# Kernel tuning notes

Hardware: AMD Instinct MI355X
Metric: run time of the kernel (lower is better)

## Reference

```python
import jax, jax.numpy as jnp
import numpy as np

N = 50000          # masked node count
E = 800000         # edges (avg degree 16)
IN_DIM, GCN_DIM, REL_DIM, TRAIN_DIM, OUT_DIM = 3, 128, 64, 128, 2
BATCHES = 1


def setup_inputs() -> dict:
    key = jax.random.key(0)
    ks = jax.random.split(key, 16)
    s = 0.05
    return {
        "features": jax.random.normal(ks[0], (N, IN_DIM), jnp.float32),
        "edge_index": jax.random.randint(ks[1], (2, E), 0, N, dtype=jnp.int32),
        "trainOT": jax.random.normal(ks[2], (TRAIN_DIM,), jnp.float32),
        "W1": jax.random.normal(ks[3], (IN_DIM, GCN_DIM), jnp.float32) * s,
        "b1": jnp.zeros((GCN_DIM,), jnp.float32),
        "W2": jax.random.normal(ks[4], (GCN_DIM, GCN_DIM), jnp.float32) * s,
        "b2": jnp.zeros((GCN_DIM,), jnp.float32),
        "Wq": jax.random.normal(ks[5], (GCN_DIM, REL_DIM), jnp.float32) * s,
        "bq": jnp.zeros((REL_DIM,), jnp.float32),
        "Wk": jax.random.normal(ks[6], (TRAIN_DIM, REL_DIM), jnp.float32) * s,
        "bk": jnp.zeros((REL_DIM,), jnp.float32),
        "Wv": jax.random.normal(ks[7], (GCN_DIM, TRAIN_DIM), jnp.float32) * s,
        "bv": jnp.zeros((TRAIN_DIM,), jnp.float32),
        "Ws": jax.random.normal(ks[8], (TRAIN_DIM, OUT_DIM * N), jnp.float32) * s,
        "bs": jnp.zeros((OUT_DIM * N,), jnp.float32),
    }


def _gcn_conv(x, W, b, src, dst, n):
    """PyG GCNConv: h = D^-1/2 (A+I) D^-1/2 (x W) + b (self-loops already in src/dst)."""
    h = x @ W                                                  # [n, d_out]
    ones = jnp.ones(src.shape[0], dtype=x.dtype)
    deg = jax.ops.segment_sum(ones, dst, num_segments=n)      # in-degree incl. self-loop
    dinv = jnp.where(deg > 0, jax.lax.rsqrt(deg), 0.0)
    norm = dinv[src] * dinv[dst]                               # [E+n]
    msg = h[src] * norm[:, None]                               # gather (dominant traffic)
    return jax.ops.segment_sum(msg, dst, num_segments=n) + b   # scatter-add


def reference(features, edge_index, trainOT, W1, b1, W2, b2, Wq, bq, Wk, bk, Wv, bv, Ws, bs):
    n = features.shape[0]
    loop = jnp.arange(n, dtype=edge_index.dtype)
    src = jnp.concatenate([edge_index[0], loop])
    dst = jnp.concatenate([edge_index[1], loop])

    h1 = jax.nn.relu(_gcn_conv(features, W1, b1, src, dst, n))   # gcn1 + relu
    h2 = _gcn_conv(h1, W2, b2, src, dst, n)                      # gcn2

    q = h2 @ Wq + bq                                             # [n, rel]
    v = h2 @ Wv + bv                                             # [n, train]
    k = trainOT @ Wk + bk                                        # [rel]
    scale = jnp.asarray(Wq.shape[1], q.dtype) ** 0.5
    rel = jax.nn.sigmoid((q @ k) / scale)                        # [n]
    summed_idea = (rel[:, None] * v).sum(axis=0)                 # [train]
    new_trainOT = trainOT + summed_idea
    speak = new_trainOT @ Ws + bs                                # [out_dim * num_nodes]
    out = speak.reshape(BATCHES, -1, OUT_DIM)
    return out, new_trainOT
```

## Files before the change

### kernel.cpp

```cpp
#include <hip/hip_runtime.h>
#include <math.h>

#define O_RPD    (0)
#define O_RPS    (256*1024)
#define O_DINV   (512*1024)
#define O_SMALL  (768*1024)
#define O_Y      (1024*1024)
#define O_RELW   (1280*1024)
#define O_REL    (1536*1024)
#define O_GHD    (1792*1024)
#define O_GHS    (2048*1024)
#define O_GOD    (2304*1024)
#define O_GOS    (2560*1024)
#define O_BSD    (2816*1024)
#define O_BSS    (2944*1024)
#define O_PART   (3072*1024)
#define O_XS     (3712*1024)
#define O_SRTD   (4608*1024)
#define O_SRTS   (11776*1024 - 3584*1024)
#define O_COLD   (11776*1024)
#define O_COLS   (15360*1024)
#define O_H1     (18688*1024)

#define NCHUNK 256
#define ZBLOCKS 1024

static __device__ __forceinline__ unsigned int f2bf(float f) {
    unsigned int u = __float_as_uint(f);
    return (u + 0x7fffu + ((u >> 16) & 1u)) >> 16;
}
static __device__ __forceinline__ float bf_lo(unsigned int w) { return __uint_as_float(w << 16); }
static __device__ __forceinline__ float bf_hi(unsigned int w) { return __uint_as_float(w & 0xffff0000u); }

static __device__ __forceinline__ int blockExclScan256(int v, volatile int* lds, int t) {
    int lane = t & 63, wid = t >> 6;
    int incl = v;
#pragma unroll
    for (int off = 1; off < 64; off <<= 1) {
        int n = __shfl_up(incl, off);
        if (lane >= off) incl += n;
    }
    if (lane == 63) lds[wid] = incl;
    __syncthreads();
    if (t == 0) {
        int s = 0;
#pragma unroll
        for (int i = 0; i < 4; ++i) { int x = lds[i]; lds[i] = s; s += x; }
    }
    __syncthreads();
    return lds[wid] + incl - v;
}

__global__ void k_hist(const int* __restrict__ eidx, int* __restrict__ ghD,
                       int* __restrict__ ghS, int E, int CS, int NB) {
    __shared__ int lh[256];
    int b = blockIdx.x, t = threadIdx.x;
    const int* arr = blockIdx.y ? eidx : (eidx + E);
    int* gh = blockIdx.y ? ghS : ghD;
    lh[t] = 0; __syncthreads();
    int s = b * CS, e = min(E, s + CS);
    for (int i = s + t; i < e; i += 256) atomicAdd(&lh[arr[i] >> 8], 1);
    __syncthreads();
    if (t < NB) gh[t * NCHUNK + b] = lh[t];
}

__global__ void k_bstart(const int* __restrict__ ghD, const int* __restrict__ ghS,
                         int* __restrict__ bsD, int* __restrict__ bsS, int NB) {
    __shared__ int lds1[4];
    __shared__ int lds2[4];
    int t = threadIdx.x;
    int vD = 0, vS = 0;
    if (t < NB) {
        const int* rD = ghD + t * NCHUNK;
        const int* rS = ghS + t * NCHUNK;
        for (int b = 0; b < NCHUNK; ++b) { vD += rD[b]; vS += rS[b]; }
    }
    int exD = blockExclScan256(vD, lds1, t);
    if (t <= NB) bsD[t] = exD;
    __syncthreads();
    int exS = blockExclScan256(vS, lds2, t);
    if (t <= NB) bsS[t] = exS;
}

__global__ void k_goff(const int* __restrict__ ghD, const int* __restrict__ ghS,
                       const int* __restrict__ bsD, const int* __restrict__ bsS,
                       int* __restrict__ goD, int* __restrict__ goS, int NB) {
    __shared__ int lds1[4];
    int nb = blockIdx.x, t = threadIdx.x;
    const int* gh = blockIdx.y ? ghS : ghD;
    const int* bs = blockIdx.y ? bsS : bsD;
    int* go = blockIdx.y ? goS : goD;
    int base = bs[nb];
    int g = gh[nb * NCHUNK + t];
    int gx = blockExclScan256(g, lds1, t);
    go[nb * NCHUNK + t] = base + gx;
}

__global__ void k_scatter(const int* __restrict__ eidx, const int* __restrict__ goD,
                          const int* __restrict__ goS, unsigned int* __restrict__ srtD,
                          unsigned int* __restrict__ srtS, int E, int CS, int NB) {
    __shared__ int lcur[256];
    int b = blockIdx.x, t = threadIdx.x;
    const int* key = blockIdx.y ? eidx : (eidx + E);
    const int* val = blockIdx.y ? (eidx + E) : eidx;
    const int* go  = blockIdx.y ? goS : goD;
    unsigned int* srt = blockIdx.y ? srtS : srtD;
    if (t < NB) lcur[t] = go[t * NCHUNK + b];
    __syncthreads();
    int s = b * CS, e = min(E, s + CS);
    for (int i = s + t; i < e; i += 256) {
        int k = key[i];
        int pos = atomicAdd(&lcur[k >> 8], 1);
        srt[pos] = ((unsigned int)(k & 255) << 16) | (unsigned int)val[i];
    }
}

__global__ void k_build(const unsigned int* __restrict__ srtD, const unsigned int* __restrict__ srtS,
                        const int* __restrict__ bsD, const int* __restrict__ bsS,
                        int* __restrict__ rpD, int* __restrict__ rpS,
                        int* __restrict__ colD, int* __restrict__ colS,
                        float* __restrict__ dinv, const float* __restrict__ x,
                        float4* __restrict__ xs4, const float* __restrict__ bs,
                        float* __restrict__ out, int N, int NB) {
    __shared__ int lcnt[256];
    __shared__ int lpos[256];
    __shared__ int lds1[4];
    int nb = blockIdx.x, t = threadIdx.x;
    bool rev = blockIdx.y != 0;
    const unsigned int* srt = rev ? srtS : srtD;
    const int* bst = rev ? bsS : bsD;
    int* rp  = rev ? rpS : rpD;
    int* col = rev ? colS : colD;
    lcnt[t] = 0; __syncthreads();
    int s = bst[nb], e = bst[nb + 1];
    for (int i = s + t; i < e; i += 256) atomicAdd(&lcnt[srt[i] >> 16], 1);
    __syncthreads();
    int c = lcnt[t];
    int cx = blockExclScan256(c, lds1, t);
    int rpv = s + cx;
    int node = (nb << 8) + t;
    rp[node] = rpv;
    lpos[t] = rpv;
    if (!rev && node < N) {
        float d = rsqrtf((float)(c + 1));
        dinv[node] = d;
        float4 v;
        v.x = x[node * 3] * d; v.y = x[node * 3 + 1] * d; v.z = x[node * 3 + 2] * d; v.w = 0.f;
        xs4[node] = v;
        reinterpret_cast<float2*>(out)[node] = reinterpret_cast<const float2*>(bs)[node];
    }
    __syncthreads();
    for (int i = s + t; i < e; i += 256) {
        unsigned int v = srt[i];
        int p = atomicAdd(&lpos[v >> 16], 1);
        col[p] = (int)(v & 0xffffu);
    }
}

__global__ void k_tiny1(const float* __restrict__ trainOT, const float* __restrict__ Wq,
                        const float* __restrict__ bq, const float* __restrict__ Wk,
                        const float* __restrict__ bk, const float* __restrict__ W2,
                        const float* __restrict__ b2, float* __restrict__ small) {
    __shared__ float kv[64];
    __shared__ float wqk[128];
    __shared__ float red[128];
    int t = threadIdx.x;
    if (t < 64) {
        float acc = bk[t];
        for (int j = 0; j < 128; ++j) acc += trainOT[j] * Wk[j * 64 + t];
        kv[t] = acc;
    }
    __syncthreads();
    float accq = 0.f;
    for (int c = 0; c < 64; ++c) accq += Wq[t * 64 + c] * kv[c];
    wqk[t] = accq;
    red[t] = (t < 64) ? bq[t] * kv[t] : 0.f;
    __syncthreads();
    for (int off = 64; off >= 1; off >>= 1) { if (t < off) red[t] += red[t + off]; __syncthreads(); }
    float bqs = red[0];
    __syncthreads();
    float acc2 = 0.f;
    for (int j = 0; j < 128; ++j) acc2 += W2[t * 128 + j] * wqk[j];
    small[t] = acc2;
    red[t] = b2[t] * wqk[t];
    __syncthreads();
    for (int off = 64; off >= 1; off >>= 1) { if (t < off) red[t] += red[t + off]; __syncthreads(); }
    if (t == 0) small[128] = bqs + red[0];
}

__global__ void k_layer1(const float4* __restrict__ xs4, const int* __restrict__ rpD,
                         const int* __restrict__ colD, const float* __restrict__ dinv,
                         const float* __restrict__ W1, const float* __restrict__ b1,
                         const float* __restrict__ small, unsigned int* __restrict__ h1s,
                         float* __restrict__ y, int N) {
    int t = threadIdx.x;
    int sub = t & 15;
    int node = blockIdx.x * 16 + (t >> 4);
    if (node >= N) return;
    float di = dinv[node];
    int s = rpD[node], e = rpD[node + 1];
    float a0 = 0.f, a1 = 0.f, a2 = 0.f;
    for (int j = s + sub; j < e; j += 16) {
        float4 xv = xs4[colD[j]];
        a0 += xv.x; a1 += xv.y; a2 += xv.z;
    }
    if (sub == 0) { float4 xv = xs4[node]; a0 += xv.x; a1 += xv.y; a2 += xv.z; }
#pragma unroll
    for (int off = 1; off < 16; off <<= 1) {
        a0 += __shfl_xor(a0, off);
        a1 += __shfl_xor(a1, off);
        a2 += __shfl_xor(a2, off);
    }
    a0 *= di; a1 *= di; a2 *= di;
    unsigned int p[4];
    float yl = 0.f;
#pragma unroll
    for (int m = 0; m < 4; ++m) {
        int c = 8 * sub + 2 * m;
        float vlo = fmaxf(a0 * W1[c]     + a1 * W1[128 + c]     + a2 * W1[256 + c]     + b1[c],     0.f) * di;
        float vhi = fmaxf(a0 * W1[c + 1] + a1 * W1[128 + c + 1] + a2 * W1[256 + c + 1] + b1[c + 1], 0.f) * di;
        p[m] = f2bf(vlo) | (f2bf(vhi) << 16);
        yl += bf_lo(p[m]) * small[c] + bf_hi(p[m]) * small[c + 1];
    }
    uint4 st; st.x = p[0]; st.y = p[1]; st.z = p[2]; st.w = p[3];
    reinterpret_cast<uint4*>(h1s + (size_t)node * 64)[sub] = st;
#pragma unroll
    for (int off = 1; off < 16; off <<= 1) yl += __shfl_xor(yl, off);
    if (sub == 0) y[node] = yl;
}

__global__ void k_dv(const float* __restrict__ y, const int* __restrict__ rpD,
                     const int* __restrict__ colD, const float* __restrict__ dinv,
                     const float* __restrict__ small, float* __restrict__ relw,
                     float* __restrict__ rel, int N) {
    int t = threadIdx.x;
    int sub = t & 15;
    int node = blockIdx.x * 16 + (t >> 4);
    if (node >= N) return;
    float di = dinv[node];
    int s = rpD[node], e = rpD[node + 1];
    float acc = (sub == 0) ? y[node] : 0.f;
    for (int j = s + sub; j < e; j += 16) acc += y[colD[j]];
#pragma unroll
    for (int off = 1; off < 16; off <<= 1) acc += __shfl_xor(acc, off);
    float z = (acc * di + small[128]) * 0.125f;
    float r = 1.f / (1.f + __expf(-z));
    if (sub == 0) { rel[node] = r; relw[node] = r * di; }
}

__global__ void k_z(const unsigned int* __restrict__ h1s, const int* __restrict__ rpS,
                    const int* __restrict__ colS, const float* __restrict__ relw,
                    const float* __restrict__ rel, float* __restrict__ part, int N) {
    int t = threadIdx.x, lane = t & 63, wid = t >> 6;
    int sub = lane & 15;
    float acc[8];
#pragma unroll
    for (int j = 0; j < 8; ++j) acc[j] = 0.f;
    float Racc = 0.f;
    for (int node = blockIdx.x * 16 + (t >> 4); node < N; node += ZBLOCKS * 16) {
        int s = rpS[node], e = rpS[node + 1];
        float w = (sub == 0) ? relw[node] : 0.f;
        for (int j = s + sub; j < e; j += 16) w += relw[colS[j]];
#pragma unroll
        for (int off = 1; off < 16; off <<= 1) w += __shfl_xor(w, off);
        uint4 v = reinterpret_cast<const uint4*>(h1s + (size_t)node * 64)[sub];
        acc[0] += w * bf_lo(v.x); acc[1] += w * bf_hi(v.x);
        acc[2] += w * bf_lo(v.y); acc[3] += w * bf_hi(v.y);
        acc[4] += w * bf_lo(v.z); acc[5] += w * bf_hi(v.z);
        acc[6] += w * bf_lo(v.w); acc[7] += w * bf_hi(v.w);
        if (sub == 0) Racc += rel[node];
    }
#pragma unroll
    for (int j = 0; j < 8; ++j) {
        acc[j] += __shfl_xor(acc[j], 16);
        acc[j] += __shfl_xor(acc[j], 32);
    }
    Racc += __shfl_xor(Racc, 16);
    Racc += __shfl_xor(Racc, 32);
    __shared__ float sS[4][132];
    if (lane < 16) {
#pragma unroll
        for (int j = 0; j < 8; ++j) sS[wid][8 * sub + j] = acc[j];
    }
    if (lane == 0) sS[wid][128] = Racc;
    __syncthreads();
    if (t < 129) part[blockIdx.x * 132 + t] = sS[0][t] + sS[1][t] + sS[2][t] + sS[3][t];
}

__global__ void k_reduce_part(const float* __restrict__ part, int nblocks, float* __restrict__ small) {
    int c = blockIdx.x;
    float acc = 0.f;
    for (int b = threadIdx.x; b < nblocks; b += blockDim.x) acc += part[b * 132 + c];
    __shared__ float sd[256];
    sd[threadIdx.x] = acc; __syncthreads();
    for (int off = 128; off; off >>= 1) { if (threadIdx.x < off) sd[threadIdx.x] += sd[threadIdx.x + off]; __syncthreads(); }
    if (threadIdx.x == 0) small[132 + c] = sd[0];
}

__global__ void k_tiny2(const float* __restrict__ trainOT, const float* __restrict__ W2,
                        const float* __restrict__ b2, const float* __restrict__ Wv,
                        const float* __restrict__ bv, float* __restrict__ small,
                        float* __restrict__ out_tail) {
    __shared__ float t1[128];
    int t = threadIdx.x;
    float R = small[260];
    float acc = R * b2[t];
    for (int j = 0; j < 128; ++j) acc += small[132 + j] * W2[j * 128 + t];
    t1[t] = acc; __syncthreads();
    float acc2 = R * bv[t];
    for (int j = 0; j < 128; ++j) acc2 += t1[j] * Wv[j * 128 + t];
    float nt = trainOT[t] + acc2;
    small[264 + t] = nt;
    out_tail[t] = nt;
}

__global__ void k_tail(const float* __restrict__ Ws, const float* __restrict__ small,
                       float* __restrict__ out, int out_n) {
    int ks = blockIdx.x & 3;
    int j = ((blockIdx.x >> 2) << 8) + threadIdx.x;
    if (j >= out_n) return;
    const float* w = Ws + (size_t)(ks * 32) * out_n + j;
    const float* nt = small + 264 + ks * 32;
    float acc = 0.f;
#pragma unroll 8
    for (int k = 0; k < 32; ++k) acc += nt[k] * w[(size_t)k * out_n];
    atomicAdd(&out[j], acc);
}

extern "C" void kernel_launch(void* const* d_in, const int* in_sizes, int n_in,
                              void* d_out, int out_size, void* d_ws, size_t ws_size,
                              hipStream_t stream) {
    const float* features = (const float*)d_in[0];
    const int*   eidx     = (const int*)d_in[1];
    const float* trainOT  = (const float*)d_in[2];
    const float* W1 = (const float*)d_in[3];
    const float* b1 = (const float*)d_in[4];
    const float* W2 = (const float*)d_in[5];
    const float* b2 = (const float*)d_in[6];
    const float* Wq = (const float*)d_in[7];
    const float* bq = (const float*)d_in[8];
    const float* Wk = (const float*)d_in[9];
    const float* bk = (const float*)d_in[10];
    const float* Wv = (const float*)d_in[11];
    const float* bv = (const float*)d_in[12];
    const float* Ws = (const float*)d_in[13];
    const float* bs = (const float*)d_in[14];

    int N = in_sizes[0] / 3;
    int E = in_sizes[1] / 2;
    int NB = (N + 255) >> 8;
    int CS = (E + NCHUNK - 1) / NCHUNK;

    char* ws = (char*)d_ws;
    int*   rpD   = (int*)(ws + O_RPD);
    int*   rpS   = (int*)(ws + O_RPS);
    float* dinv  = (float*)(ws + O_DINV);
    float* small = (float*)(ws + O_SMALL);
    float* y     = (float*)(ws + O_Y);
    float* relw  = (float*)(ws + O_RELW);
    float* rel   = (float*)(ws + O_REL);
    int*   ghD   = (int*)(ws + O_GHD);
    int*   ghS   = (int*)(ws + O_GHS);
    int*   goD   = (int*)(ws + O_GOD);
    int*   goS   = (int*)(ws + O_GOS);
    int*   bsD   = (int*)(ws + O_BSD);
    int*   bsS   = (int*)(ws + O_BSS);
    float* part  = (float*)(ws + O_PART);
    float4* xs4  = (float4*)(ws + O_XS);
    unsigned int* srtD = (unsigned int*)(ws + O_SRTD);
    unsigned int* srtS = (unsigned int*)(ws + O_SRTS);
    int*   colD  = (int*)(ws + O_COLD);
    int*   colS  = (int*)(ws + O_COLS);
    unsigned int* h1s = (unsigned int*)(ws + O_H1);
    float* out   = (float*)d_out;
    int out_n = out_size - 128;

    k_tiny1<<<1, 128, 0, stream>>>(trainOT, Wq, bq, Wk, bk, W2, b2, small);
    k_hist<<<dim3(NCHUNK, 2), 256, 0, stream>>>(eidx, ghD, ghS, E, CS, NB);
    k_bstart<<<1, 256, 0, stream>>>(ghD, ghS, bsD, bsS, NB);
    k_goff<<<dim3(NB, 2), 256, 0, stream>>>(ghD, ghS, bsD, bsS, goD, goS, NB);
    k_scatter<<<dim3(NCHUNK, 2), 256, 0, stream>>>(eidx, goD, goS, srtD, srtS, E, CS, NB);
    k_build<<<dim3(NB, 2), 256, 0, stream>>>(srtD, srtS, bsD, bsS, rpD, rpS, colD, colS,
                                             dinv, features, xs4, bs, out, N, NB);
    k_layer1<<<(N + 15) / 16, 256, 0, stream>>>(xs4, rpD, colD, dinv, W1, b1, small, h1s, y, N);
    k_dv<<<(N + 15) / 16, 256, 0, stream>>>(y, rpD, colD, dinv, small, relw, rel, N);
    k_z<<<ZBLOCKS, 256, 0, stream>>>(h1s, rpS, colS, relw, rel, part, N);
    k_reduce_part<<<129, 256, 0, stream>>>(part, ZBLOCKS, small);
    k_tiny2<<<1, 128, 0, stream>>>(trainOT, W2, b2, Wv, bv, small, out + out_n);
    k_tail<<<((out_n + 255) / 256) * 4, 256, 0, stream>>>(Ws, small, out, out_n);
}
```

Measured before the change: 113.0 us.

## Aggregate directly from bucket-sorted edges with LDS atomics, dropping CSR build

Removes the per-node CSR construction (row pointers and column arrays) and instead aggregates over the 256-node bucket-sorted edge lists with shared-memory atomics per block. The bf16 h1 buffer is no longer stored. Layer-1 activations are recomputed from a compact per-node float4 of pre-activation inputs and dinv. The separate partial-reduce kernel is folded into k_tiny2, and the rel sum moves into k_dv. This cuts global traffic and launches, at the cost of LDS atomic contention, recomputing h1, and a serial reduction over blocks in a single-block kernel.

```diff
diff --git a/kernel.cpp b/kernel.cpp
--- a/kernel.cpp
+++ b/kernel.cpp
@@ -1,36 +1,23 @@
 #include <hip/hip_runtime.h>
 #include <math.h>
 
-#define O_RPD    (0)
-#define O_RPS    (256*1024)
-#define O_DINV   (512*1024)
-#define O_SMALL  (768*1024)
-#define O_Y      (1024*1024)
-#define O_RELW   (1280*1024)
-#define O_REL    (1536*1024)
-#define O_GHD    (1792*1024)
-#define O_GHS    (2048*1024)
-#define O_GOD    (2304*1024)
-#define O_GOS    (2560*1024)
-#define O_BSD    (2816*1024)
-#define O_BSS    (2944*1024)
-#define O_PART   (3072*1024)
-#define O_XS     (3712*1024)
-#define O_SRTD   (4608*1024)
-#define O_SRTS   (11776*1024 - 3584*1024)
-#define O_COLD   (11776*1024)
-#define O_COLS   (15360*1024)
-#define O_H1     (18688*1024)
+#define O_SMALL  (0)
+#define O_DINV   (256*1024)
+#define O_Y      (512*1024)
+#define O_RELW   (768*1024)
+#define O_PART   (1024*1024)
+#define O_GHD    (1536*1024)
+#define O_GHS    (1792*1024)
+#define O_GOD    (2048*1024)
+#define O_GOS    (2304*1024)
+#define O_BSD    (2560*1024)
+#define O_BSS    (2688*1024)
+#define O_XS     (2816*1024)
+#define O_G1     (3840*1024)
+#define O_SRTD   (4864*1024)
+#define O_SRTS   (8192*1024)
 
 #define NCHUNK 256
-#define ZBLOCKS 1024
-
-static __device__ __forceinline__ unsigned int f2bf(float f) {
-    unsigned int u = __float_as_uint(f);
-    return (u + 0x7fffu + ((u >> 16) & 1u)) >> 16;
-}
-static __device__ __forceinline__ float bf_lo(unsigned int w) { return __uint_as_float(w << 16); }
-static __device__ __forceinline__ float bf_hi(unsigned int w) { return __uint_as_float(w & 0xffff0000u); }
 
 static __device__ __forceinline__ int blockExclScan256(int v, volatile int* lds, int t) {
     int lane = t & 63, wid = t >> 6;
@@ -115,45 +102,24 @@
     }
 }
 
-__global__ void k_build(const unsigned int* __restrict__ srtD, const unsigned int* __restrict__ srtS,
-                        const int* __restrict__ bsD, const int* __restrict__ bsS,
-                        int* __restrict__ rpD, int* __restrict__ rpS,
-                        int* __restrict__ colD, int* __restrict__ colS,
-                        float* __restrict__ dinv, const float* __restrict__ x,
-                        float4* __restrict__ xs4, const float* __restrict__ bs,
-                        float* __restrict__ out, int N, int NB) {
+__global__ void k_prep(const unsigned int* __restrict__ srtD, const int* __restrict__ bsD,
+                       const float* __restrict__ x, const float* __restrict__ bs,
+                       float* __restrict__ out, float* __restrict__ dinv,
+                       float4* __restrict__ xs4, int N) {
     __shared__ int lcnt[256];
-    __shared__ int lpos[256];
-    __shared__ int lds1[4];
-    int nb = blockIdx.x, t = threadIdx.x;
-    bool rev = blockIdx.y != 0;
-    const unsigned int* srt = rev ? srtS : srtD;
-    const int* bst = rev ? bsS : bsD;
-    int* rp  = rev ? rpS : rpD;
-    int* col = rev ? colS : colD;
+    int nb = blockIdx.x, t = threadIdx.x;
     lcnt[t] = 0; __syncthreads();
-    int s = bst[nb], e = bst[nb + 1];
-    for (int i = s + t; i < e; i += 256) atomicAdd(&lcnt[srt[i] >> 16], 1);
-    __syncthreads();
-    int c = lcnt[t];
-    int cx = blockExclScan256(c, lds1, t);
-    int rpv = s + cx;
+    int s = bsD[nb], e = bsD[nb + 1];
+    for (int i = s + t; i < e; i += 256) atomicAdd(&lcnt[srtD[i] >> 16], 1);
+    __syncthreads();
     int node = (nb << 8) + t;
-    rp[node] = rpv;
-    lpos[t] = rpv;
-    if (!rev && node < N) {
-        float d = rsqrtf((float)(c + 1));
+    if (node < N) {
+        float d = rsqrtf((float)(lcnt[t] + 1));
         dinv[node] = d;
         float4 v;
         v.x = x[node * 3] * d; v.y = x[node * 3 + 1] * d; v.z = x[node * 3 + 2] * d; v.w = 0.f;
         xs4[node] = v;
         reinterpret_cast<float2*>(out)[node] = reinterpret_cast<const float2*>(bs)[node];
-    }
-    __syncthreads();
-    for (int i = s + t; i < e; i += 256) {
-        unsigned int v = srt[i];
-        int p = atomicAdd(&lpos[v >> 16], 1);
-        col[p] = (int)(v & 0xffffu);
     }
 }
 
@@ -188,124 +154,155 @@
     if (t == 0) small[128] = bqs + red[0];
 }
 
-__global__ void k_layer1(const float4* __restrict__ xs4, const int* __restrict__ rpD,
-                         const int* __restrict__ colD, const float* __restrict__ dinv,
-                         const float* __restrict__ W1, const float* __restrict__ b1,
-                         const float* __restrict__ small, unsigned int* __restrict__ h1s,
-                         float* __restrict__ y, int N) {
-    int t = threadIdx.x;
-    int sub = t & 15;
-    int node = blockIdx.x * 16 + (t >> 4);
-    if (node >= N) return;
-    float di = dinv[node];
-    int s = rpD[node], e = rpD[node + 1];
-    float a0 = 0.f, a1 = 0.f, a2 = 0.f;
-    for (int j = s + sub; j < e; j += 16) {
-        float4 xv = xs4[colD[j]];
-        a0 += xv.x; a1 += xv.y; a2 += xv.z;
-    }
-    if (sub == 0) { float4 xv = xs4[node]; a0 += xv.x; a1 += xv.y; a2 += xv.z; }
-#pragma unroll
-    for (int off = 1; off < 16; off <<= 1) {
-        a0 += __shfl_xor(a0, off);
-        a1 += __shfl_xor(a1, off);
-        a2 += __shfl_xor(a2, off);
-    }
-    a0 *= di; a1 *= di; a2 *= di;
-    unsigned int p[4];
-    float yl = 0.f;
-#pragma unroll
-    for (int m = 0; m < 4; ++m) {
-        int c = 8 * sub + 2 * m;
-        float vlo = fmaxf(a0 * W1[c]     + a1 * W1[128 + c]     + a2 * W1[256 + c]     + b1[c],     0.f) * di;
-        float vhi = fmaxf(a0 * W1[c + 1] + a1 * W1[128 + c + 1] + a2 * W1[256 + c + 1] + b1[c + 1], 0.f) * di;
-        p[m] = f2bf(vlo) | (f2bf(vhi) << 16);
-        yl += bf_lo(p[m]) * small[c] + bf_hi(p[m]) * small[c + 1];
-    }
-    uint4 st; st.x = p[0]; st.y = p[1]; st.z = p[2]; st.w = p[3];
-    reinterpret_cast<uint4*>(h1s + (size_t)node * 64)[sub] = st;
-#pragma unroll
-    for (int off = 1; off < 16; off <<= 1) yl += __shfl_xor(yl, off);
-    if (sub == 0) y[node] = yl;
-}
-
-__global__ void k_dv(const float* __restrict__ y, const int* __restrict__ rpD,
-                     const int* __restrict__ colD, const float* __restrict__ dinv,
+__global__ void k_y(const unsigned int* __restrict__ srtD, const int* __restrict__ bsD,
+                    const float4* __restrict__ xs4, const float* __restrict__ dinv,
+                    const float* __restrict__ W1, const float* __restrict__ b1,
+                    const float* __restrict__ small, float4* __restrict__ g1,
+                    float* __restrict__ y, int N) {
+    __shared__ float ax[256], ay[256], az[256];
+    __shared__ float W1s[384];
+    __shared__ float b1s[128], wqks[128];
+    int nb = blockIdx.x, t = threadIdx.x;
+    ax[t] = 0.f; ay[t] = 0.f; az[t] = 0.f;
+    if (t < 128) { W1s[t] = W1[t]; W1s[128 + t] = W1[128 + t]; W1s[256 + t] = W1[256 + t];
+                   b1s[t] = b1[t]; wqks[t] = small[t]; }
+    __syncthreads();
+    int s = bsD[nb], e = bsD[nb + 1];
+    for (int i = s + t; i < e; i += 256) {
+        unsigned int v = srtD[i];
+        int d = v >> 16;
+        float4 xv = xs4[v & 0xffffu];
+        atomicAdd(&ax[d], xv.x); atomicAdd(&ay[d], xv.y); atomicAdd(&az[d], xv.z);
+    }
+    __syncthreads();
+    int grp = t >> 4, sub = t & 15;
+#pragma unroll 4
+    for (int r = 0; r < 16; ++r) {
+        int nl = r * 16 + grp;
+        int node = (nb << 8) + nl;
+        float a0 = 0.f, a1 = 0.f, a2 = 0.f, di = 0.f, yl = 0.f;
+        if (node < N) {
+            di = dinv[node];
+            float4 self = xs4[node];
+            a0 = (ax[nl] + self.x) * di;
+            a1 = (ay[nl] + self.y) * di;
+            a2 = (az[nl] + self.z) * di;
+#pragma unroll
+            for (int m = 0; m < 8; ++m) {
+                int c = sub * 8 + m;
+                float h = fmaxf(a0 * W1s[c] + a1 * W1s[128 + c] + a2 * W1s[256 + c] + b1s[c], 0.f);
+                yl += h * wqks[c];
+            }
+        }
+#pragma unroll
+        for (int off = 1; off < 16; off <<= 1) yl += __shfl_xor(yl, off);
+        if (node < N && sub == 0) {
+            y[node] = yl * di;
+            float4 gv; gv.x = a0; gv.y = a1; gv.z = a2; gv.w = di;
+            g1[node] = gv;
+        }
+    }
+}
+
+__global__ void k_dv(const unsigned int* __restrict__ srtD, const int* __restrict__ bsD,
+                     const float* __restrict__ y, const float* __restrict__ dinv,
                      const float* __restrict__ small, float* __restrict__ relw,
-                     float* __restrict__ rel, int N) {
-    int t = threadIdx.x;
-    int sub = t & 15;
-    int node = blockIdx.x * 16 + (t >> 4);
-    if (node >= N) return;
-    float di = dinv[node];
-    int s = rpD[node], e = rpD[node + 1];
-    float acc = (sub == 0) ? y[node] : 0.f;
-    for (int j = s + sub; j < e; j += 16) acc += y[colD[j]];
-#pragma unroll
-    for (int off = 1; off < 16; off <<= 1) acc += __shfl_xor(acc, off);
-    float z = (acc * di + small[128]) * 0.125f;
-    float r = 1.f / (1.f + __expf(-z));
-    if (sub == 0) { rel[node] = r; relw[node] = r * di; }
-}
-
-__global__ void k_z(const unsigned int* __restrict__ h1s, const int* __restrict__ rpS,
-                    const int* __restrict__ colS, const float* __restrict__ relw,
-                    const float* __restrict__ rel, float* __restrict__ part, int N) {
-    int t = threadIdx.x, lane = t & 63, wid = t >> 6;
-    int sub = lane & 15;
+                     float* __restrict__ part, int N) {
+    __shared__ float dvl[256];
+    __shared__ float red[256];
+    int nb = blockIdx.x, t = threadIdx.x;
+    dvl[t] = 0.f; __syncthreads();
+    int s = bsD[nb], e = bsD[nb + 1];
+    float bias = small[128];
+    for (int i = s + t; i < e; i += 256) {
+        unsigned int v = srtD[i];
+        atomicAdd(&dvl[v >> 16], y[v & 0xffffu]);
+    }
+    __syncthreads();
+    int node = (nb << 8) + t;
+    float rel = 0.f;
+    if (node < N) {
+        float di = dinv[node];
+        float dv = (dvl[t] + y[node]) * di;
+        float z = (dv + bias) * 0.125f;
+        rel = 1.f / (1.f + __expf(-z));
+        relw[node] = rel * di;
+    }
+    red[t] = rel; __syncthreads();
+    for (int off = 128; off >= 1; off >>= 1) { if (t < off) red[t] += red[t + off]; __syncthreads(); }
+    if (t == 0) part[nb * 132 + 128] = red[0];
+}
+
+__global__ void k_S(const unsigned int* __restrict__ srtS, const int* __restrict__ bsS,
+                    const float* __restrict__ relw, const float4* __restrict__ g1,
+                    const float* __restrict__ W1, const float* __restrict__ b1,
+                    float* __restrict__ part, int N) {
+    __shared__ float zl[256];
+    __shared__ float W1s[384];
+    __shared__ float b1s[128];
+    __shared__ float sS[4][128];
+    int nb = blockIdx.x, t = threadIdx.x;
+    zl[t] = 0.f;
+    if (t < 128) { W1s[t] = W1[t]; W1s[128 + t] = W1[128 + t]; W1s[256 + t] = W1[256 + t];
+                   b1s[t] = b1[t]; }
+    __syncthreads();
+    int s = bsS[nb], e = bsS[nb + 1];
+    for (int i = s + t; i < e; i += 256) {
+        unsigned int v = srtS[i];
+        atomicAdd(&zl[v >> 16], relw[v & 0xffffu]);
+    }
+    __syncthreads();
+    int grp = t >> 4, sub = t & 15, lane = t & 63, wid = t >> 6;
     float acc[8];
 #pragma unroll
-    for (int j = 0; j < 8; ++j) acc[j] = 0.f;
-    float Racc = 0.f;
-    for (int node = blockIdx.x * 16 + (t >> 4); node < N; node += ZBLOCKS * 16) {
-        int s = rpS[node], e = rpS[node + 1];
-        float w = (sub == 0) ? relw[node] : 0.f;
-        for (int j = s + sub; j < e; j += 16) w += relw[colS[j]];
-#pragma unroll
-        for (int off = 1; off < 16; off <<= 1) w += __shfl_xor(w, off);
-        uint4 v = reinterpret_cast<const uint4*>(h1s + (size_t)node * 64)[sub];
-        acc[0] += w * bf_lo(v.x); acc[1] += w * bf_hi(v.x);
-        acc[2] += w * bf_lo(v.y); acc[3] += w * bf_hi(v.y);
-        acc[4] += w * bf_lo(v.z); acc[5] += w * bf_hi(v.z);
-        acc[6] += w * bf_lo(v.w); acc[7] += w * bf_hi(v.w);
-        if (sub == 0) Racc += rel[node];
-    }
-#pragma unroll
-    for (int j = 0; j < 8; ++j) {
-        acc[j] += __shfl_xor(acc[j], 16);
-        acc[j] += __shfl_xor(acc[j], 32);
-    }
-    Racc += __shfl_xor(Racc, 16);
-    Racc += __shfl_xor(Racc, 32);
-    __shared__ float sS[4][132];
+    for (int m = 0; m < 8; ++m) acc[m] = 0.f;
+#pragma unroll 4
+    for (int r = 0; r < 16; ++r) {
+        int nl = r * 16 + grp;
+        int node = (nb << 8) + nl;
+        if (node < N) {
+            float4 gv = g1[node];
+            float zu = zl[nl] + relw[node];
+            float zw = zu * gv.w;
+#pragma unroll
+            for (int m = 0; m < 8; ++m) {
+                int c = sub * 8 + m;
+                float h = fmaxf(gv.x * W1s[c] + gv.y * W1s[128 + c] + gv.z * W1s[256 + c] + b1s[c], 0.f);
+                acc[m] += zw * h;
+            }
+        }
+    }
+#pragma unroll
+    for (int m = 0; m < 8; ++m) {
+        acc[m] += __shfl_xor(acc[m], 16);
+        acc[m] += __shfl_xor(acc[m], 32);
+    }
     if (lane < 16) {
 #pragma unroll
-        for (int j = 0; j < 8; ++j) sS[wid][8 * sub + j] = acc[j];
-    }
-    if (lane == 0) sS[wid][128] = Racc;
-    __syncthreads();
-    if (t < 129) part[blockIdx.x * 132 + t] = sS[0][t] + sS[1][t] + sS[2][t] + sS[3][t];
-}
-
-__global__ void k_reduce_part(const float* __restrict__ part, int nblocks, float* __restrict__ small) {
-    int c = blockIdx.x;
-    float acc = 0.f;
-    for (int b = threadIdx.x; b < nblocks; b += blockDim.x) acc += part[b * 132 + c];
-    __shared__ float sd[256];
-    sd[threadIdx.x] = acc; __syncthreads();
-    for (int off = 128; off; off >>= 1) { if (threadIdx.x < off) sd[threadIdx.x] += sd[threadIdx.x + off]; __syncthreads(); }
-    if (threadIdx.x == 0) small[132 + c] = sd[0];
+        for (int m = 0; m < 8; ++m) sS[wid][lane * 8 + m] = acc[m];
+    }
+    __syncthreads();
+    if (t < 128) part[nb * 132 + t] = sS[0][t] + sS[1][t] + sS[2][t] + sS[3][t];
 }
 
 __global__ void k_tiny2(const float* __restrict__ trainOT, const float* __restrict__ W2,
                         const float* __restrict__ b2, const float* __restrict__ Wv,
-                        const float* __restrict__ bv, float* __restrict__ small,
-                        float* __restrict__ out_tail) {
+                        const float* __restrict__ bv, const float* __restrict__ part,
+                        float* __restrict__ small, float* __restrict__ out_tail, int NB) {
+    __shared__ float Ss[128];
     __shared__ float t1[128];
+    __shared__ float red[128];
     int t = threadIdx.x;
-    float R = small[260];
+    float sv = 0.f;
+    for (int b = 0; b < NB; ++b) sv += part[b * 132 + t];
+    Ss[t] = sv;
+    float r = 0.f;
+    for (int b = t; b < NB; b += 128) r += part[b * 132 + 128];
+    red[t] = r; __syncthreads();
+    for (int off = 64; off >= 1; off >>= 1) { if (t < off) red[t] += red[t + off]; __syncthreads(); }
+    float R = red[0];
     float acc = R * b2[t];
-    for (int j = 0; j < 128; ++j) acc += small[132 + j] * W2[j * 128 + t];
+    for (int j = 0; j < 128; ++j) acc += Ss[j] * W2[j * 128 + t];
     t1[t] = acc; __syncthreads();
     float acc2 = R * bv[t];
     for (int j = 0; j < 128; ++j) acc2 += t1[j] * Wv[j * 128 + t];
@@ -352,26 +349,21 @@
     int CS = (E + NCHUNK - 1) / NCHUNK;
 
     char* ws = (char*)d_ws;
-    int*   rpD   = (int*)(ws + O_RPD);
-    int*   rpS   = (int*)(ws + O_RPS);
+    float* small = (float*)(ws + O_SMALL);
     float* dinv  = (float*)(ws + O_DINV);
-    float* small = (float*)(ws + O_SMALL);
     float* y     = (float*)(ws + O_Y);
     float* relw  = (float*)(ws + O_RELW);
-    float* rel   = (float*)(ws + O_REL);
+    float* part  = (float*)(ws + O_PART);
     int*   ghD   = (int*)(ws + O_GHD);
     int*   ghS   = (int*)(ws + O_GHS);
     int*   goD   = (int*)(ws + O_GOD);
     int*   goS   = (int*)(ws + O_GOS);
     int*   bsD   = (int*)(ws + O_BSD);
     int*   bsS   = (int*)(ws + O_BSS);
-    float* part  = (float*)(ws + O_PART);
     float4* xs4  = (float4*)(ws + O_XS);
+    float4* g1   = (float4*)(ws + O_G1);
     unsigned int* srtD = (unsigned int*)(ws + O_SRTD);
     unsigned int* srtS = (unsigned int*)(ws + O_SRTS);
-    int*   colD  = (int*)(ws + O_COLD);
-    int*   colS  = (int*)(ws + O_COLS);
-    unsigned int* h1s = (unsigned int*)(ws + O_H1);
     float* out   = (float*)d_out;
     int out_n = out_size - 128;
 
@@ -380,12 +372,10 @@
     k_bstart<<<1, 256, 0, stream>>>(ghD, ghS, bsD, bsS, NB);
     k_goff<<<dim3(NB, 2), 256, 0, stream>>>(ghD, ghS, bsD, bsS, goD, goS, NB);
     k_scatter<<<dim3(NCHUNK, 2), 256, 0, stream>>>(eidx, goD, goS, srtD, srtS, E, CS, NB);
-    k_build<<<dim3(NB, 2), 256, 0, stream>>>(srtD, srtS, bsD, bsS, rpD, rpS, colD, colS,
-                                             dinv, features, xs4, bs, out, N, NB);
-    k_layer1<<<(N + 15) / 16, 256, 0, stream>>>(xs4, rpD, colD, dinv, W1, b1, small, h1s, y, N);
-    k_dv<<<(N + 15) / 16, 256, 0, stream>>>(y, rpD, colD, dinv, small, relw, rel, N);
-    k_z<<<ZBLOCKS, 256, 0, stream>>>(h1s, rpS, colS, relw, rel, part, N);
-    k_reduce_part<<<129, 256, 0, stream>>>(part, ZBLOCKS, small);
-    k_tiny2<<<1, 128, 0, stream>>>(trainOT, W2, b2, Wv, bv, small, out + out_n);
+    k_prep<<<NB, 256, 0, stream>>>(srtD, bsD, features, bs, out, dinv, xs4, N);
+    k_y<<<NB, 256, 0, stream>>>(srtD, bsD, xs4, dinv, W1, b1, small, g1, y, N);
+    k_dv<<<NB, 256, 0, stream>>>(srtD, bsD, y, dinv, small, relw, part, N);
+    k_S<<<NB, 256, 0, stream>>>(srtS, bsS, relw, g1, W1, b1, part, N);
+    k_tiny2<<<1, 128, 0, stream>>>(trainOT, W2, b2, Wv, bv, part, small, out + out_n, NB);
     k_tail<<<((out_n + 255) / 256) * 4, 256, 0, stream>>>(Ws, small, out, out_n);
 }
```

Result: slower. 172.2 us (+52.4%).

## Recompute layer-1 activations in k_z instead of storing bf16 h1

Applied to the files above, without the earlier changes.

Instead of materialising the 128-wide bf16 h1 matrix per node, layer-1 stores only the aggregated 3-dim input plus dinv as a float4, and k_z recomputes relu(xW1+b1) on the fly from W1/b1 held in shared memory. This removes a large intermediate write and read (about 256 bytes per node) in exchange for extra ALU work in k_z, and it also drops the bf16 rounding. Separately, the single-block tiny matvec kernel is widened from 128 to 1024 threads, splitting the K dimension into slices and reducing through shared memory.

```diff
diff --git a/kernel.cpp b/kernel.cpp
--- a/kernel.cpp
+++ b/kernel.cpp
@@ -16,21 +16,14 @@
 #define O_BSS    (2944*1024)
 #define O_PART   (3072*1024)
 #define O_XS     (3712*1024)
-#define O_SRTD   (4608*1024)
-#define O_SRTS   (11776*1024 - 3584*1024)
-#define O_COLD   (11776*1024)
-#define O_COLS   (15360*1024)
-#define O_H1     (18688*1024)
+#define O_G1     (4608*1024)
+#define O_SRTD   (5632*1024)
+#define O_SRTS   (9216*1024)
+#define O_COLD   (12544*1024)
+#define O_COLS   (16128*1024)
 
 #define NCHUNK 256
 #define ZBLOCKS 1024
-
-static __device__ __forceinline__ unsigned int f2bf(float f) {
-    unsigned int u = __float_as_uint(f);
-    return (u + 0x7fffu + ((u >> 16) & 1u)) >> 16;
-}
-static __device__ __forceinline__ float bf_lo(unsigned int w) { return __uint_as_float(w << 16); }
-static __device__ __forceinline__ float bf_hi(unsigned int w) { return __uint_as_float(w & 0xffff0000u); }
 
 static __device__ __forceinline__ int blockExclScan256(int v, volatile int* lds, int t) {
     int lane = t & 63, wid = t >> 6;
@@ -188,11 +181,11 @@
     if (t == 0) small[128] = bqs + red[0];
 }
 
-__global__ void k_layer1(const float4* __restrict__ xs4, const int* __restrict__ rpD,
-                         const int* __restrict__ colD, const float* __restrict__ dinv,
-                         const float* __restrict__ W1, const float* __restrict__ b1,
-                         const float* __restrict__ small, unsigned int* __restrict__ h1s,
-                         float* __restrict__ y, int N) {
+__global__ void k_y(const float4* __restrict__ xs4, const int* __restrict__ rpD,
+                    const int* __restrict__ colD, const float* __restrict__ dinv,
+                    const float* __restrict__ W1, const float* __restrict__ b1,
+                    const float* __restrict__ small, float4* __restrict__ g1,
+                    float* __restrict__ y, int N) {
     int t = threadIdx.x;
     int sub = t & 15;
     int node = blockIdx.x * 16 + (t >> 4);
@@ -212,21 +205,20 @@
         a2 += __shfl_xor(a2, off);
     }
     a0 *= di; a1 *= di; a2 *= di;
-    unsigned int p[4];
     float yl = 0.f;
 #pragma unroll
-    for (int m = 0; m < 4; ++m) {
-        int c = 8 * sub + 2 * m;
-        float vlo = fmaxf(a0 * W1[c]     + a1 * W1[128 + c]     + a2 * W1[256 + c]     + b1[c],     0.f) * di;
-        float vhi = fmaxf(a0 * W1[c + 1] + a1 * W1[128 + c + 1] + a2 * W1[256 + c + 1] + b1[c + 1], 0.f) * di;
-        p[m] = f2bf(vlo) | (f2bf(vhi) << 16);
-        yl += bf_lo(p[m]) * small[c] + bf_hi(p[m]) * small[c + 1];
-    }
-    uint4 st; st.x = p[0]; st.y = p[1]; st.z = p[2]; st.w = p[3];
-    reinterpret_cast<uint4*>(h1s + (size_t)node * 64)[sub] = st;
+    for (int m = 0; m < 8; ++m) {
+        int c = sub * 8 + m;
+        float h = fmaxf(a0 * W1[c] + a1 * W1[128 + c] + a2 * W1[256 + c] + b1[c], 0.f);
+        yl += h * small[c];
+    }
 #pragma unroll
     for (int off = 1; off < 16; off <<= 1) yl += __shfl_xor(yl, off);
-    if (sub == 0) y[node] = yl;
+    if (sub == 0) {
+        y[node] = yl * di;
+        float4 gv; gv.x = a0; gv.y = a1; gv.z = a2; gv.w = di;
+        g1[node] = gv;
+    }
 }
 
 __global__ void k_dv(const float* __restrict__ y, const int* __restrict__ rpD,
@@ -248,14 +240,21 @@
     if (sub == 0) { rel[node] = r; relw[node] = r * di; }
 }
 
-__global__ void k_z(const unsigned int* __restrict__ h1s, const int* __restrict__ rpS,
+__global__ void k_z(const float4* __restrict__ g1, const int* __restrict__ rpS,
                     const int* __restrict__ colS, const float* __restrict__ relw,
-                    const float* __restrict__ rel, float* __restrict__ part, int N) {
+                    const float* __restrict__ rel, const float* __restrict__ W1,
+                    const float* __restrict__ b1, float* __restrict__ part, int N) {
+    __shared__ float W1s[384];
+    __shared__ float b1s[128];
+    __shared__ float sS[4][132];
     int t = threadIdx.x, lane = t & 63, wid = t >> 6;
     int sub = lane & 15;
+    if (t < 128) { W1s[t] = W1[t]; W1s[128 + t] = W1[128 + t]; W1s[256 + t] = W1[256 + t];
+                   b1s[t] = b1[t]; }
+    __syncthreads();
     float acc[8];
 #pragma unroll
-    for (int j = 0; j < 8; ++j) acc[j] = 0.f;
+    for (int m = 0; m < 8; ++m) acc[m] = 0.f;
     float Racc = 0.f;
     for (int node = blockIdx.x * 16 + (t >> 4); node < N; node += ZBLOCKS * 16) {
         int s = rpS[node], e = rpS[node + 1];
@@ -263,24 +262,26 @@
         for (int j = s + sub; j < e; j += 16) w += relw[colS[j]];
 #pragma unroll
         for (int off = 1; off < 16; off <<= 1) w += __shfl_xor(w, off);
-        uint4 v = reinterpret_cast<const uint4*>(h1s + (size_t)node * 64)[sub];
-        acc[0] += w * bf_lo(v.x); acc[1] += w * bf_hi(v.x);
-        acc[2] += w * bf_lo(v.y); acc[3] += w * bf_hi(v.y);
-        acc[4] += w * bf_lo(v.z); acc[5] += w * bf_hi(v.z);
-        acc[6] += w * bf_lo(v.w); acc[7] += w * bf_hi(v.w);
+        float4 gv = g1[node];
+        float zw = w * gv.w;
+#pragma unroll
+        for (int m = 0; m < 8; ++m) {
+            int c = sub * 8 + m;
+            float h = fmaxf(gv.x * W1s[c] + gv.y * W1s[128 + c] + gv.z * W1s[256 + c] + b1s[c], 0.f);
+            acc[m] += zw * h;
+        }
         if (sub == 0) Racc += rel[node];
     }
 #pragma unroll
-    for (int j = 0; j < 8; ++j) {
-        acc[j] += __shfl_xor(acc[j], 16);
-        acc[j] += __shfl_xor(acc[j], 32);
+    for (int m = 0; m < 8; ++m) {
+        acc[m] += __shfl_xor(acc[m], 16);
+        acc[m] += __shfl_xor(acc[m], 32);
     }
     Racc += __shfl_xor(Racc, 16);
     Racc += __shfl_xor(Racc, 32);
-    __shared__ float sS[4][132];
     if (lane < 16) {
 #pragma unroll
-        for (int j = 0; j < 8; ++j) sS[wid][8 * sub + j] = acc[j];
+        for (int m = 0; m < 8; ++m) sS[wid][sub * 8 + m] = acc[m];
     }
     if (lane == 0) sS[wid][128] = Racc;
     __syncthreads();
@@ -297,21 +298,41 @@
     if (threadIdx.x == 0) small[132 + c] = sd[0];
 }
 
-__global__ void k_tiny2(const float* __restrict__ trainOT, const float* __restrict__ W2,
-                        const float* __restrict__ b2, const float* __restrict__ Wv,
-                        const float* __restrict__ bv, float* __restrict__ small,
-                        float* __restrict__ out_tail) {
+__global__ void k_tinytail(const float* __restrict__ trainOT, const float* __restrict__ W2,
+                           const float* __restrict__ b2, const float* __restrict__ Wv,
+                           const float* __restrict__ bv, float* __restrict__ small,
+                           float* __restrict__ out_tail) {
+    __shared__ float partial[1024];
+    __shared__ float Ss[128];
     __shared__ float t1[128];
     int t = threadIdx.x;
+    int o = t & 127, sl = t >> 7;
+    if (t < 128) Ss[t] = small[132 + t];
+    __syncthreads();
     float R = small[260];
-    float acc = R * b2[t];
-    for (int j = 0; j < 128; ++j) acc += small[132 + j] * W2[j * 128 + t];
-    t1[t] = acc; __syncthreads();
-    float acc2 = R * bv[t];
-    for (int j = 0; j < 128; ++j) acc2 += t1[j] * Wv[j * 128 + t];
-    float nt = trainOT[t] + acc2;
-    small[264 + t] = nt;
-    out_tail[t] = nt;
+    float acc = 0.f;
+#pragma unroll
+    for (int j = sl * 16; j < sl * 16 + 16; ++j) acc += Ss[j] * W2[j * 128 + o];
+    partial[t] = acc; __syncthreads();
+    if (t < 128) {
+        float v = R * b2[t];
+#pragma unroll
+        for (int k = 0; k < 8; ++k) v += partial[t + 128 * k];
+        t1[t] = v;
+    }
+    __syncthreads();
+    float acc2 = 0.f;
+#pragma unroll
+    for (int j = sl * 16; j < sl * 16 + 16; ++j) acc2 += t1[j] * Wv[j * 128 + o];
+    partial[t] = acc2; __syncthreads();
+    if (t < 128) {
+        float v = R * bv[t];
+#pragma unroll
+        for (int k = 0; k < 8; ++k) v += partial[t + 128 * k];
+        float nt = trainOT[t] + v;
+        small[264 + t] = nt;
+        out_tail[t] = nt;
+    }
 }
 
 __global__ void k_tail(const float* __restrict__ Ws, const float* __restrict__ small,
@@ -367,11 +388,11 @@
     int*   bsS   = (int*)(ws + O_BSS);
     float* part  = (float*)(ws + O_PART);
     float4* xs4  = (float4*)(ws + O_XS);
+    float4* g1   = (float4*)(ws + O_G1);
     unsigned int* srtD = (unsigned int*)(ws + O_SRTD);
     unsigned int* srtS = (unsigned int*)(ws + O_SRTS);
     int*   colD  = (int*)(ws + O_COLD);
     int*   colS  = (int*)(ws + O_COLS);
-    unsigned int* h1s = (unsigned int*)(ws + O_H1);
     float* out   = (float*)d_out;
     int out_n = out_size - 128;
 
@@ -382,10 +403,10 @@
     k_scatter<<<dim3(NCHUNK, 2), 256, 0, stream>>>(eidx, goD, goS, srtD, srtS, E, CS, NB);
     k_build<<<dim3(NB, 2), 256, 0, stream>>>(srtD, srtS, bsD, bsS, rpD, rpS, colD, colS,
                                              dinv, features, xs4, bs, out, N, NB);
-    k_layer1<<<(N + 15) / 16, 256, 0, stream>>>(xs4, rpD, colD, dinv, W1, b1, small, h1s, y, N);
+    k_y<<<(N + 15) / 16, 256, 0, stream>>>(xs4, rpD, colD, dinv, W1, b1, small, g1, y, N);
     k_dv<<<(N + 15) / 16, 256, 0, stream>>>(y, rpD, colD, dinv, small, relw, rel, N);
-    k_z<<<ZBLOCKS, 256, 0, stream>>>(h1s, rpS, colS, relw, rel, part, N);
+    k_z<<<ZBLOCKS, 256, 0, stream>>>(g1, rpS, colS, relw, rel, W1, b1, part, N);
     k_reduce_part<<<129, 256, 0, stream>>>(part, ZBLOCKS, small);
-    k_tiny2<<<1, 128, 0, stream>>>(trainOT, W2, b2, Wv, bv, small, out + out_n);
+    k_tinytail<<<1, 1024, 0, stream>>>(trainOT, W2, b2, Wv, bv, small, out + out_n);
     k_tail<<<((out_n + 255) / 256) * 4, 256, 0, stream>>>(Ws, small, out, out_n);
 }
```

Result: faster. 108.7 us (-3.8%).
